# Kernel optimization log

Measured on AMD Instinct MI355X. Metric: run time of the kernel, lower is better.

The kernel has to match this reference:

```python
import jax, jax.numpy as jnp
import numpy as np

EPS = 1e-10
B, S, D, K = 8, 2048, 512, 1024
TEMP = 1.0  # quantizer temperature set to 1.0 in SQVAE.__init__


def _ln(x, g, b):
    m = x.mean(-1, keepdims=True)
    v = x.var(-1, keepdims=True)
    return (x - m) / jnp.sqrt(v + 1e-5) * g + b


def _mlp(x, w1, b1, g1, be1, w2, b2, g2, be2):
    # feed_forward: Linear -> ReLU -> LayerNorm, twice (MLPLayers=2)
    h = _ln(jax.nn.relu(x @ w1 + b1), g1, be1)
    return _ln(jax.nn.relu(h @ w2 + b2), g2, be2)


def setup_inputs() -> dict:
    key = jax.random.key(0)
    ks = jax.random.split(key, 20)
    W = 0.04  # small init scale to keep distances / softmax well-conditioned
    p = lambda k, sh, s=1.0: jax.random.normal(k, sh, dtype=jnp.float32) * s
    return {
        'x': p(ks[0], (B, S, D)),
        'gumbel_u': jax.random.uniform(ks[1], (B * S, K), dtype=jnp.float32),
        'enc_w1': p(ks[2], (D, D), W), 'enc_b1': jnp.zeros(D, jnp.float32),
        'enc_g1': jnp.ones(D, jnp.float32), 'enc_be1': jnp.zeros(D, jnp.float32),
        'enc_w2': p(ks[3], (D, D), W), 'enc_b2': jnp.zeros(D, jnp.float32),
        'enc_g2': jnp.ones(D, jnp.float32), 'enc_be2': jnp.zeros(D, jnp.float32),
        'dec_w1': p(ks[4], (D, D), W), 'dec_b1': jnp.zeros(D, jnp.float32),
        'dec_g1': jnp.ones(D, jnp.float32), 'dec_be1': jnp.zeros(D, jnp.float32),
        'dec_w2': p(ks[5], (D, D), W), 'dec_b2': jnp.zeros(D, jnp.float32),
        'dec_g2': jnp.ones(D, jnp.float32), 'dec_be2': jnp.zeros(D, jnp.float32),
        'codebook': p(ks[6], (K, D)),
        'log_param_q': jnp.zeros((), jnp.float32),
    }


def reference(x, gumbel_u, enc_w1, enc_b1, enc_g1, enc_be1, enc_w2, enc_b2, enc_g2, enc_be2,
              dec_w1, dec_b1, dec_g1, dec_be1, dec_w2, dec_b2, dec_g2, dec_be2,
              codebook, log_param_q):
    bs, seq, d = x.shape
    z = _mlp(x, enc_w1, enc_b1, enc_g1, enc_be1, enc_w2, enc_b2, enc_g2, enc_be2)
    # gaussian_1: log_var_q = 0 -> var_q = exp(log_param_q_scalar)
    var_q = jnp.exp(log_param_q)
    w = 0.5 / jnp.clip(var_q, 1e-10)  # 0.5 * precision_q (scalar)
    zf = z.reshape(-1, d)  # [N, D]
    # cdist^2 style distance, scaled by weight -> logits [N, K]
    dist = w * (jnp.sum(zf * zf, axis=1, keepdims=True)
                + jnp.sum(codebook * codebook, axis=1)
                - 2.0 * zf @ codebook.T)
    logit = -dist
    logp = jax.nn.log_softmax(logit, axis=-1)
    probs = jnp.exp(logp)
    # gumbel-softmax sample (train path), noise provided as uniform input
    g = -jnp.log(-jnp.log(gumbel_u + EPS) + EPS)
    encodings = jax.nn.softmax((logit + g) / TEMP, axis=-1)
    z_q = (encodings @ codebook).reshape(bs, seq, d)
    kld_discrete = jnp.sum(probs * logp) / bs
    kld_continuous = jnp.mean(jnp.sum((z - z_q) ** 2 * w, axis=(1, 2)))
    loss = kld_discrete + kld_continuous
    avg_probs = jnp.mean(jax.lax.stop_gradient(probs), axis=0)
    perplexity = jnp.exp(-jnp.sum(avg_probs * jnp.log(avg_probs + 1e-7)))
    x_rec = _mlp(z_q, dec_w1, dec_b1, dec_g1, dec_be1, dec_w2, dec_b2, dec_g2, dec_be2)
    return x_rec, loss, perplexity
```

## Files before the change

kernel.cpp:

```cpp
#include <hip/hip_runtime.h>
#include <math.h>

#define NROWS 16384
#define DIM   512
#define KCODE 1024

typedef __attribute__((ext_vector_type(8))) __bf16 bf16x8;
typedef __attribute__((ext_vector_type(4))) float f32x4;

__device__ __forceinline__ float wave_reduce_sum(float v) {
  #pragma unroll
  for (int m = 1; m < 64; m <<= 1) v += __shfl_xor(v, m, 64);
  return v;
}
__device__ __forceinline__ float wave_reduce_max(float v) {
  #pragma unroll
  for (int m = 1; m < 64; m <<= 1) v = fmaxf(v, __shfl_xor(v, m, 64));
  return v;
}
__device__ __forceinline__ unsigned short f2bf(float f) {
  union { float f; unsigned u; } v; v.f = f;
  unsigned r = v.u + 0x7FFFu + ((v.u >> 16) & 1u);
  return (unsigned short)(r >> 16);
}
__device__ __forceinline__ float bf2f(unsigned short h) {
  union { unsigned u; float f; } v; v.u = ((unsigned)h) << 16;
  return v.f;
}
__device__ __forceinline__ uint4 pack8(const float* x) {
  uint4 r;
  r.x = (unsigned)f2bf(x[0]) | ((unsigned)f2bf(x[1]) << 16);
  r.y = (unsigned)f2bf(x[2]) | ((unsigned)f2bf(x[3]) << 16);
  r.z = (unsigned)f2bf(x[4]) | ((unsigned)f2bf(x[5]) << 16);
  r.w = (unsigned)f2bf(x[6]) | ((unsigned)f2bf(x[7]) << 16);
  return r;
}

__device__ __forceinline__ void glds16(const void* g, void* lds) {
  __builtin_amdgcn_global_load_lds(
      (const __attribute__((address_space(1))) unsigned int*)g,
      (__attribute__((address_space(3))) unsigned int*)lds, 16, 0, 0);
}

template <int NPASS, int EPI, int K, int N, int LDA>
__global__ __launch_bounds__(256) void gemm_bt(
    const unsigned short* A0, const unsigned short* A1, const unsigned short* A2,
    const unsigned short* B0, const unsigned short* B1, const unsigned short* B2,
    const float* __restrict__ bias,
    const float* __restrict__ znorm, const float* __restrict__ cnorm,
    const float* __restrict__ lpq,
    const unsigned short* __restrict__ zh, const unsigned short* __restrict__ zl,
    float* __restrict__ kldc,
    unsigned short* __restrict__ outb, float* __restrict__ outf) {
  __shared__ char smem[17408];
  unsigned short* Abuf = (unsigned short*)smem;
  unsigned short* Bbuf = (unsigned short*)(smem + 8192);
  const int t = threadIdx.x;
  const int l = t & 63, w = t >> 6;
  const int wm = w >> 1, wn = w & 1;
  const int NTN = N / 128;
  const int b = blockIdx.x;
  const int xcd = b & 7;
  const int j = b >> 3;
  const int m0 = (xcd * 16 + j / NTN) * 128;
  const int n0 = (j % NTN) * 128;

  f32x4 acc[4][4];
  #pragma unroll
  for (int i = 0; i < 4; ++i)
    #pragma unroll
    for (int jj = 0; jj < 4; ++jj) acc[i][jj] = (f32x4){0.f, 0.f, 0.f, 0.f};

  const int row_lo = w * 16 + (l & 15);
  const int row_hi = (w + 4) * 16 + (l & 15);
  const int kcol = (l >> 4) * 8;
  char* ldsA0 = (char*)Abuf + w * 1024;
  char* ldsA1 = (char*)Abuf + (w + 4) * 1024;
  char* ldsB0 = (char*)Bbuf + w * 1024;
  char* ldsB1 = (char*)Bbuf + (w + 4) * 1024;

  const unsigned short* APs[3] = {A0, A1, A2};
  const unsigned short* BPs[3] = {B0, B1, B2};

  #pragma unroll 1
  for (int p = 0; p < NPASS; ++p) {
    const unsigned short* aA0 = APs[p] + (size_t)(m0 + row_lo) * LDA + kcol;
    const unsigned short* aA1 = APs[p] + (size_t)(m0 + row_hi) * LDA + kcol;
    const unsigned short* aB0 = BPs[p] + (size_t)(n0 + row_lo) * K + kcol;
    const unsigned short* aB1 = BPs[p] + (size_t)(n0 + row_hi) * K + kcol;
    for (int kt = 0; kt < K; kt += 32) {
      glds16(aA0 + kt, ldsA0);
      glds16(aA1 + kt, ldsA1);
      glds16(aB0 + kt, ldsB0);
      glds16(aB1 + kt, ldsB1);
      __syncthreads();
      bf16x8 af[4], bfr[4];
      #pragma unroll
      for (int i = 0; i < 4; ++i) {
        af[i]  = *(const bf16x8*)&Abuf[((wm * 4 + i) * 64 + l) * 8];
        bfr[i] = *(const bf16x8*)&Bbuf[((wn * 4 + i) * 64 + l) * 8];
      }
      #pragma unroll
      for (int mi = 0; mi < 4; ++mi)
        #pragma unroll
        for (int ni = 0; ni < 4; ++ni)
          acc[mi][ni] = __builtin_amdgcn_mfma_f32_16x16x32_bf16(af[mi], bfr[ni], acc[mi][ni], 0, 0, 0);
      __syncthreads();
    }
  }

  float* slab = (float*)(smem + w * 4352);
  const int q = l >> 4, c16 = l & 15;
  const int rr = l >> 4, c4 = (l & 15) * 4;
  const float wq = (EPI >= 1) ? 0.5f / fmaxf(expf(lpq[0]), 1e-10f) : 0.f;
  float local = 0.f;

  #pragma unroll
  for (int mi = 0; mi < 4; ++mi) {
    __syncthreads();
    #pragma unroll
    for (int ni = 0; ni < 4; ++ni)
      #pragma unroll
      for (int r = 0; r < 4; ++r)
        slab[(q * 4 + r) * 68 + ni * 16 + c16] = acc[mi][ni][r];
    __syncthreads();
    #pragma unroll
    for (int pp = 0; pp < 4; ++pp) {
      const int row = pp * 4 + rr;
      const float4 v4 = *(const float4*)&slab[row * 68 + c4];
      float v[4] = {v4.x, v4.y, v4.z, v4.w};
      const int m = m0 + wm * 64 + mi * 16 + row;
      const int nc = n0 + wn * 64 + c4;
      if (EPI == 0) {
        const float4 b4 = *(const float4*)&bias[nc];
        v[0] = fmaxf(v[0] + b4.x, 0.f);
        v[1] = fmaxf(v[1] + b4.y, 0.f);
        v[2] = fmaxf(v[2] + b4.z, 0.f);
        v[3] = fmaxf(v[3] + b4.w, 0.f);
        uint2 st;
        st.x = (unsigned)f2bf(v[0]) | ((unsigned)f2bf(v[1]) << 16);
        st.y = (unsigned)f2bf(v[2]) | ((unsigned)f2bf(v[3]) << 16);
        *(uint2*)&outb[(size_t)m * N + nc] = st;
      } else if (EPI == 1) {
        const float zn = znorm[m];
        const float4 cn = *(const float4*)&cnorm[nc];
        float4 o;
        o.x = -wq * (zn + cn.x - 2.f * v[0]);
        o.y = -wq * (zn + cn.y - 2.f * v[1]);
        o.z = -wq * (zn + cn.z - 2.f * v[2]);
        o.w = -wq * (zn + cn.w - 2.f * v[3]);
        *(float4*)&outf[(size_t)m * N + nc] = o;
      } else {
        const uint2 h2 = *(const uint2*)&zh[(size_t)m * N + nc];
        const uint2 l2 = *(const uint2*)&zl[(size_t)m * N + nc];
        const float z0 = bf2f((unsigned short)(h2.x & 0xFFFF)) + bf2f((unsigned short)(l2.x & 0xFFFF));
        const float z1 = bf2f((unsigned short)(h2.x >> 16))    + bf2f((unsigned short)(l2.x >> 16));
        const float z2 = bf2f((unsigned short)(h2.y & 0xFFFF)) + bf2f((unsigned short)(l2.y & 0xFFFF));
        const float z3 = bf2f((unsigned short)(h2.y >> 16))    + bf2f((unsigned short)(l2.y >> 16));
        const float d0 = z0 - v[0], d1 = z1 - v[1], d2 = z2 - v[2], d3 = z3 - v[3];
        local += d0 * d0 + d1 * d1 + d2 * d2 + d3 * d3;
        uint2 st;
        st.x = (unsigned)f2bf(v[0]) | ((unsigned)f2bf(v[1]) << 16);
        st.y = (unsigned)f2bf(v[2]) | ((unsigned)f2bf(v[3]) << 16);
        *(uint2*)&outb[(size_t)m * N + nc] = st;
      }
    }
  }
  if (EPI == 2) {
    local = wave_reduce_sum(local) * wq;
    if (l == 0) atomicAdd(kldc, local);
  }
}

template <int MODE>
__global__ __launch_bounds__(256) void ln_rows(
    const unsigned short* __restrict__ X, const float* __restrict__ g,
    const float* __restrict__ be, unsigned short* __restrict__ Y,
    unsigned short* __restrict__ Yl, float* __restrict__ znorm,
    float* __restrict__ Yf) {
  const int l = threadIdx.x & 63, wv = threadIdx.x >> 6;
  float gv[8], bv[8];
  {
    const float4 a = *(const float4*)&g[l * 8];
    const float4 b = *(const float4*)&g[l * 8 + 4];
    gv[0] = a.x; gv[1] = a.y; gv[2] = a.z; gv[3] = a.w;
    gv[4] = b.x; gv[5] = b.y; gv[6] = b.z; gv[7] = b.w;
    const float4 c = *(const float4*)&be[l * 8];
    const float4 d = *(const float4*)&be[l * 8 + 4];
    bv[0] = c.x; bv[1] = c.y; bv[2] = c.z; bv[3] = c.w;
    bv[4] = d.x; bv[5] = d.y; bv[6] = d.z; bv[7] = d.w;
  }
  const int row0 = blockIdx.x * 32 + wv * 8;
  for (int rr = 0; rr < 8; ++rr) {
    const int row = row0 + rr;
    const uint4 raw = *(const uint4*)&X[(size_t)row * 512 + l * 8];
    float v[8];
    const unsigned rw[4] = {raw.x, raw.y, raw.z, raw.w};
    #pragma unroll
    for (int i = 0; i < 4; ++i) {
      v[2 * i]     = bf2f((unsigned short)(rw[i] & 0xFFFF));
      v[2 * i + 1] = bf2f((unsigned short)(rw[i] >> 16));
    }
    float s = 0.f, ss = 0.f;
    #pragma unroll
    for (int i = 0; i < 8; ++i) { s += v[i]; ss += v[i] * v[i]; }
    #pragma unroll
    for (int m = 1; m < 64; m <<= 1) {
      s += __shfl_xor(s, m, 64);
      ss += __shfl_xor(ss, m, 64);
    }
    const float mean = s * (1.f / 512.f);
    const float var = ss * (1.f / 512.f) - mean * mean;
    const float rstd = rsqrtf(var + 1e-5f);
    float y[8];
    #pragma unroll
    for (int i = 0; i < 8; ++i) y[i] = (v[i] - mean) * rstd * gv[i] + bv[i];
    if (MODE == 0) {
      *(uint4*)&Y[(size_t)row * 512 + l * 8] = pack8(y);
    } else if (MODE == 1) {
      float lo[8], ns = 0.f;
      unsigned short hx[8];
      #pragma unroll
      for (int i = 0; i < 8; ++i) {
        hx[i] = f2bf(y[i]);
        lo[i] = y[i] - bf2f(hx[i]);
        ns += y[i] * y[i];
      }
      uint4 hv;
      hv.x = (unsigned)hx[0] | ((unsigned)hx[1] << 16);
      hv.y = (unsigned)hx[2] | ((unsigned)hx[3] << 16);
      hv.z = (unsigned)hx[4] | ((unsigned)hx[5] << 16);
      hv.w = (unsigned)hx[6] | ((unsigned)hx[7] << 16);
      *(uint4*)&Y[(size_t)row * 512 + l * 8] = hv;
      *(uint4*)&Yl[(size_t)row * 512 + l * 8] = pack8(lo);
      ns = wave_reduce_sum(ns);
      if (l == 0) znorm[row] = ns;
    } else {
      float4 o0, o1;
      o0.x = y[0]; o0.y = y[1]; o0.z = y[2]; o0.w = y[3];
      o1.x = y[4]; o1.y = y[5]; o1.z = y[6]; o1.w = y[7];
      *(float4*)&Yf[(size_t)row * 512 + l * 8] = o0;
      *(float4*)&Yf[(size_t)row * 512 + l * 8 + 4] = o1;
    }
  }
}

__global__ __launch_bounds__(256) void convert_f32_bf16(
    const float* __restrict__ X, unsigned short* __restrict__ Y) {
  const size_t i = ((size_t)blockIdx.x * 256 + threadIdx.x) * 8;
  const float4 a = *(const float4*)&X[i];
  const float4 b = *(const float4*)&X[i + 4];
  float v[8] = {a.x, a.y, a.z, a.w, b.x, b.y, b.z, b.w};
  *(uint4*)&Y[i] = pack8(v);
}

__global__ __launch_bounds__(256) void prep_cb(
    const float* __restrict__ CB, unsigned short* __restrict__ H,
    unsigned short* __restrict__ L, float* __restrict__ cnorm) {
  const int wv = threadIdx.x >> 6, l = threadIdx.x & 63;
  const int r = blockIdx.x * 4 + wv;
  const float* row = &CB[(size_t)r * 512 + l * 8];
  const float4 a = *(const float4*)row;
  const float4 b = *(const float4*)(row + 4);
  float x[8] = {a.x, a.y, a.z, a.w, b.x, b.y, b.z, b.w};
  float s = 0.f, lo[8];
  unsigned short hi[8];
  #pragma unroll
  for (int i = 0; i < 8; ++i) {
    s += x[i] * x[i];
    hi[i] = f2bf(x[i]);
    lo[i] = x[i] - bf2f(hi[i]);
  }
  uint4 hv;
  hv.x = (unsigned)hi[0] | ((unsigned)hi[1] << 16);
  hv.y = (unsigned)hi[2] | ((unsigned)hi[3] << 16);
  hv.z = (unsigned)hi[4] | ((unsigned)hi[5] << 16);
  hv.w = (unsigned)hi[6] | ((unsigned)hi[7] << 16);
  *(uint4*)&H[(size_t)r * 512 + l * 8] = hv;
  *(uint4*)&L[(size_t)r * 512 + l * 8] = pack8(lo);
  s = wave_reduce_sum(s);
  if (l == 0) cnorm[r] = s;
}

__global__ __launch_bounds__(256) void transpose_f32_bf16(
    const float* __restrict__ in, unsigned short* __restrict__ out, int R, int C) {
  __shared__ float tile[32][33];
  const int ntc = C >> 5;
  const int c0 = (blockIdx.x % ntc) * 32, r0 = (blockIdx.x / ntc) * 32;
  const int tx = threadIdx.x & 31, ty = threadIdx.x >> 5;
  #pragma unroll
  for (int i = 0; i < 4; ++i)
    tile[ty + 8 * i][tx] = in[(size_t)(r0 + ty + 8 * i) * C + c0 + tx];
  __syncthreads();
  #pragma unroll
  for (int i = 0; i < 4; ++i)
    out[(size_t)(c0 + ty + 8 * i) * R + r0 + tx] = f2bf(tile[tx][ty + 8 * i]);
}

__global__ __launch_bounds__(256) void softmax_gumbel(
    const float* logits, const float* __restrict__ U, unsigned short* E,
    float* __restrict__ colsum, float* __restrict__ kldd_acc) {
  __shared__ float cs[1024];
  __shared__ float kd[4];
  const int t = threadIdx.x;
  const int wv = t >> 6, l = t & 63;
  #pragma unroll
  for (int i = 0; i < 4; ++i) cs[t + 256 * i] = 0.f;
  __syncthreads();
  float psum[16];
  #pragma unroll
  for (int i = 0; i < 16; ++i) psum[i] = 0.f;
  float kldd = 0.f;
  const int nbase = blockIdx.x * 16 + wv * 4;

  for (int it = 0; it < 4; ++it) {
    const int row = nbase + it;
    const size_t off = (size_t)row * KCODE + 4 * l;
    float v[16];
    #pragma unroll
    for (int jj = 0; jj < 4; ++jj) {
      const float4 t4 = *(const float4*)&logits[off + 256 * jj];
      v[4 * jj + 0] = t4.x; v[4 * jj + 1] = t4.y; v[4 * jj + 2] = t4.z; v[4 * jj + 3] = t4.w;
    }
    float m = v[0];
    #pragma unroll
    for (int i = 1; i < 16; ++i) m = fmaxf(m, v[i]);
    m = wave_reduce_max(m);
    float se = 0.f;
    #pragma unroll
    for (int i = 0; i < 16; ++i) se += expf(v[i] - m);
    se = wave_reduce_sum(se);
    const float lz = logf(se);
    float pl = 0.f;
    #pragma unroll
    for (int i = 0; i < 16; ++i) {
      const float lp = v[i] - m - lz;
      const float p = expf(lp);
      psum[i] += p;
      pl += p * lp;
    }
    kldd += pl;
    float y[16];
    #pragma unroll
    for (int jj = 0; jj < 4; ++jj) {
      const float4 t4 = *(const float4*)&U[off + 256 * jj];
      y[4 * jj + 0] = v[4 * jj + 0] - logf(-logf(t4.x + 1e-10f) + 1e-10f);
      y[4 * jj + 1] = v[4 * jj + 1] - logf(-logf(t4.y + 1e-10f) + 1e-10f);
      y[4 * jj + 2] = v[4 * jj + 2] - logf(-logf(t4.z + 1e-10f) + 1e-10f);
      y[4 * jj + 3] = v[4 * jj + 3] - logf(-logf(t4.w + 1e-10f) + 1e-10f);
    }
    float m2 = y[0];
    #pragma unroll
    for (int i = 1; i < 16; ++i) m2 = fmaxf(m2, y[i]);
    m2 = wave_reduce_max(m2);
    float s2 = 0.f;
    #pragma unroll
    for (int i = 0; i < 16; ++i) s2 += expf(y[i] - m2);
    s2 = wave_reduce_sum(s2);
    const float inv = 1.f / s2;
    #pragma unroll
    for (int jj = 0; jj < 4; ++jj) {
      ushort4 e;
      e.x = f2bf(expf(y[4 * jj + 0] - m2) * inv);
      e.y = f2bf(expf(y[4 * jj + 1] - m2) * inv);
      e.z = f2bf(expf(y[4 * jj + 2] - m2) * inv);
      e.w = f2bf(expf(y[4 * jj + 3] - m2) * inv);
      *(ushort4*)&E[(size_t)row * 2048 + 4 * l + 256 * jj] = e;
    }
  }
  #pragma unroll
  for (int jj = 0; jj < 4; ++jj)
    #pragma unroll
    for (int c = 0; c < 4; ++c)
      atomicAdd(&cs[256 * jj + 4 * l + c], psum[4 * jj + c]);
  kldd = wave_reduce_sum(kldd);
  if (l == 0) kd[wv] = kldd;
  __syncthreads();
  #pragma unroll
  for (int i = 0; i < 4; ++i) {
    const float vv = cs[t + 256 * i];
    if (vv != 0.f) atomicAdd(&colsum[t + 256 * i], vv);
  }
  if (t == 0) atomicAdd(kldd_acc, kd[0] + kd[1] + kd[2] + kd[3]);
}

__global__ __launch_bounds__(256) void finalize(
    const float* __restrict__ colsum, const float* __restrict__ scal,
    float* __restrict__ out) {
  const int t = threadIdx.x;
  float ent = 0.f;
  #pragma unroll
  for (int jj = 0; jj < 4; ++jj) {
    const float a = colsum[t + 256 * jj] * (1.f / 16384.f);
    ent += a * logf(a + 1e-7f);
  }
  ent = wave_reduce_sum(ent);
  __shared__ float red[4];
  if ((t & 63) == 0) red[t >> 6] = ent;
  __syncthreads();
  if (t == 0) {
    const float tot = red[0] + red[1] + red[2] + red[3];
    out[0] = (scal[0] + scal[1]) * (1.f / 8.f);
    out[1] = expf(-tot);
  }
}

extern "C" void kernel_launch(void* const* d_in, const int* in_sizes, int n_in,
                              void* d_out, int out_size, void* d_ws, size_t ws_size,
                              hipStream_t stream) {
  const float* x      = (const float*)d_in[0];
  const float* gu     = (const float*)d_in[1];
  const float* enc_w1 = (const float*)d_in[2];
  const float* enc_b1 = (const float*)d_in[3];
  const float* enc_g1 = (const float*)d_in[4];
  const float* enc_e1 = (const float*)d_in[5];
  const float* enc_w2 = (const float*)d_in[6];
  const float* enc_b2 = (const float*)d_in[7];
  const float* enc_g2 = (const float*)d_in[8];
  const float* enc_e2 = (const float*)d_in[9];
  const float* dec_w1 = (const float*)d_in[10];
  const float* dec_b1 = (const float*)d_in[11];
  const float* dec_g1 = (const float*)d_in[12];
  const float* dec_e1 = (const float*)d_in[13];
  const float* dec_w2 = (const float*)d_in[14];
  const float* dec_b2 = (const float*)d_in[15];
  const float* dec_g2 = (const float*)d_in[16];
  const float* dec_e2 = (const float*)d_in[17];
  const float* cb     = (const float*)d_in[18];
  const float* lpq    = (const float*)d_in[19];
  float* out = (float*)d_out;
  char* wsb = (char*)d_ws;

  float*          logits = (float*)(wsb + 0);
  unsigned short* Eb     = (unsigned short*)(wsb + 0);
  unsigned short* t1     = (unsigned short*)(wsb + 67108864);
  unsigned short* xb     = (unsigned short*)(wsb + 83886080);
  unsigned short* zh     = xb;
  unsigned short* hq     = (unsigned short*)(wsb + 100663296);
  unsigned short* zl     = (unsigned short*)(wsb + 117440512);
  unsigned short* wt0    = (unsigned short*)(wsb + 134217728);
  unsigned short* wt1    = wt0 + 262144;
  unsigned short* wt2    = wt1 + 262144;
  unsigned short* wt3    = wt2 + 262144;
  unsigned short* cbh    = (unsigned short*)(wsb + 136314880);
  unsigned short* cbl    = (unsigned short*)(wsb + 137363456);
  unsigned short* cbT    = (unsigned short*)(wsb + 138412032);
  float*          znorm  = (float*)(wsb + 139460608);
  float*          cnorm  = (float*)(wsb + 139526144);
  float*          colsum = (float*)(wsb + 139530240);
  float*          scal   = (float*)(wsb + 139534336);

  hipMemsetAsync(colsum, 0, 4096 + 16, stream);

  convert_f32_bf16<<<4096, 256, 0, stream>>>(x, xb);
  prep_cb<<<256, 256, 0, stream>>>(cb, cbh, cbl, cnorm);
  transpose_f32_bf16<<<256, 256, 0, stream>>>(enc_w1, wt0, 512, 512);
  transpose_f32_bf16<<<256, 256, 0, stream>>>(enc_w2, wt1, 512, 512);
  transpose_f32_bf16<<<256, 256, 0, stream>>>(dec_w1, wt2, 512, 512);
  transpose_f32_bf16<<<256, 256, 0, stream>>>(dec_w2, wt3, 512, 512);
  transpose_f32_bf16<<<512, 256, 0, stream>>>(cb, cbT, 1024, 512);

  gemm_bt<1, 0, 512, 512, 512><<<512, 256, 0, stream>>>(
      xb, nullptr, nullptr, wt0, nullptr, nullptr, enc_b1,
      nullptr, nullptr, nullptr, nullptr, nullptr, nullptr, t1, nullptr);
  ln_rows<0><<<512, 256, 0, stream>>>(t1, enc_g1, enc_e1, hq, nullptr, nullptr, nullptr);
  gemm_bt<1, 0, 512, 512, 512><<<512, 256, 0, stream>>>(
      hq, nullptr, nullptr, wt1, nullptr, nullptr, enc_b2,
      nullptr, nullptr, nullptr, nullptr, nullptr, nullptr, t1, nullptr);
  ln_rows<1><<<512, 256, 0, stream>>>(t1, enc_g2, enc_e2, zh, zl, znorm, nullptr);
  gemm_bt<3, 1, 512, 1024, 512><<<1024, 256, 0, stream>>>(
      zh, zl, zh, cbh, cbh, cbl, nullptr,
      znorm, cnorm, lpq, nullptr, nullptr, nullptr, nullptr, logits);
  softmax_gumbel<<<1024, 256, 0, stream>>>(logits, gu, Eb, colsum, &scal[0]);
  gemm_bt<1, 2, 1024, 512, 2048><<<512, 256, 0, stream>>>(
      Eb, nullptr, nullptr, cbT, nullptr, nullptr, nullptr,
      nullptr, nullptr, lpq, zh, zl, &scal[1], hq, nullptr);
  gemm_bt<1, 0, 512, 512, 512><<<512, 256, 0, stream>>>(
      hq, nullptr, nullptr, wt2, nullptr, nullptr, dec_b1,
      nullptr, nullptr, nullptr, nullptr, nullptr, nullptr, t1, nullptr);
  ln_rows<0><<<512, 256, 0, stream>>>(t1, dec_g1, dec_e1, zl, nullptr, nullptr, nullptr);
  gemm_bt<1, 0, 512, 512, 512><<<512, 256, 0, stream>>>(
      zl, nullptr, nullptr, wt3, nullptr, nullptr, dec_b2,
      nullptr, nullptr, nullptr, nullptr, nullptr, nullptr, t1, nullptr);
  ln_rows<2><<<512, 256, 0, stream>>>(t1, dec_g2, dec_e2, nullptr, nullptr, nullptr, out);
  finalize<<<1, 256, 0, stream>>>(colsum, scal, out + 8388608);
}
```

Measured before the change: 537.3 us.

## Double-buffer LDS tiles in bf16 GEMM to overlap global loads with MFMA

Doubles the GEMM shared-memory allocation into two 16 KB stages. The first K-tile is preloaded before the loop, and each iteration issues the async global-to-LDS loads for the next tile before computing on the current one. This removes the barrier that used to sit between loading and computing each tile, so load latency can be hidden behind the MFMA work. The cost is twice the LDS per block, which may lower occupancy, plus extra address arithmetic.

```diff
diff --git a/kernel.cpp b/kernel.cpp
--- a/kernel.cpp
+++ b/kernel.cpp
@@ -52,9 +52,7 @@
     const unsigned short* __restrict__ zh, const unsigned short* __restrict__ zl,
     float* __restrict__ kldc,
     unsigned short* __restrict__ outb, float* __restrict__ outf) {
-  __shared__ char smem[17408];
-  unsigned short* Abuf = (unsigned short*)smem;
-  unsigned short* Bbuf = (unsigned short*)(smem + 8192);
+  __shared__ char smem[32768];
   const int t = threadIdx.x;
   const int l = t & 63, w = t >> 6;
   const int wm = w >> 1, wn = w & 1;
@@ -74,10 +72,10 @@
   const int row_lo = w * 16 + (l & 15);
   const int row_hi = (w + 4) * 16 + (l & 15);
   const int kcol = (l >> 4) * 8;
-  char* ldsA0 = (char*)Abuf + w * 1024;
-  char* ldsA1 = (char*)Abuf + (w + 4) * 1024;
-  char* ldsB0 = (char*)Bbuf + w * 1024;
-  char* ldsB1 = (char*)Bbuf + (w + 4) * 1024;
+  const int dA0 = w * 1024;
+  const int dA1 = (w + 4) * 1024;
+  const int dB0 = 8192 + w * 1024;
+  const int dB1 = 8192 + (w + 4) * 1024;
 
   const unsigned short* APs[3] = {A0, A1, A2};
   const unsigned short* BPs[3] = {B0, B1, B2};
@@ -88,17 +86,29 @@
     const unsigned short* aA1 = APs[p] + (size_t)(m0 + row_hi) * LDA + kcol;
     const unsigned short* aB0 = BPs[p] + (size_t)(n0 + row_lo) * K + kcol;
     const unsigned short* aB1 = BPs[p] + (size_t)(n0 + row_hi) * K + kcol;
+    glds16(aA0, smem + dA0);
+    glds16(aA1, smem + dA1);
+    glds16(aB0, smem + dB0);
+    glds16(aB1, smem + dB1);
+    __syncthreads();
+    #pragma unroll 1
     for (int kt = 0; kt < K; kt += 32) {
-      glds16(aA0 + kt, ldsA0);
-      glds16(aA1 + kt, ldsA1);
-      glds16(aB0 + kt, ldsB0);
-      glds16(aB1 + kt, ldsB1);
-      __syncthreads();
+      const int cur = (kt >> 5) & 1;
+      const int nxt = cur ^ 1;
+      if (kt + 32 < K) {
+        char* nb = smem + nxt * 16384;
+        glds16(aA0 + kt + 32, nb + dA0);
+        glds16(aA1 + kt + 32, nb + dA1);
+        glds16(aB0 + kt + 32, nb + dB0);
+        glds16(aB1 + kt + 32, nb + dB1);
+      }
+      const unsigned short* Ab = (const unsigned short*)(smem + cur * 16384);
+      const unsigned short* Bb = (const unsigned short*)(smem + cur * 16384 + 8192);
       bf16x8 af[4], bfr[4];
       #pragma unroll
       for (int i = 0; i < 4; ++i) {
-        af[i]  = *(const bf16x8*)&Abuf[((wm * 4 + i) * 64 + l) * 8];
-        bfr[i] = *(const bf16x8*)&Bbuf[((wn * 4 + i) * 64 + l) * 8];
+        af[i]  = *(const bf16x8*)&Ab[((wm * 4 + i) * 64 + l) * 8];
+        bfr[i] = *(const bf16x8*)&Bb[((wn * 4 + i) * 64 + l) * 8];
       }
       #pragma unroll
       for (int mi = 0; mi < 4; ++mi)
```

Result: no change. 529.9 us (-1.4%).
